# Kernel optimization log

Hardware: AMD Instinct MI355X
Metric: run time of the kernel (lower is better)

## Reference

```python
import jax, jax.numpy as jnp
import numpy as np

K_SIZE = 7  # kernel_size (odd)


def setup_inputs() -> dict:
    key = jax.random.key(0)
    k0, k1, k2, k3 = jax.random.split(key, 4)
    B, C, H, W = 4, 128, 192, 192
    O, K = 128, K_SIZE
    x = jax.random.normal(k0, (B, C, H, W), dtype=jnp.float32)
    offsets = jax.random.normal(k1, (B, K, H, W), dtype=jnp.float32) * 0.5
    tumor_center = jax.random.uniform(k2, (B, 2), dtype=jnp.float32) * H  # (h, w) coords
    kernel_w = jax.random.normal(k3, (O * K, C), dtype=jnp.float32) / np.sqrt(C)  # 1x1 conv weight
    kernel_b = jnp.zeros((O * K,), dtype=jnp.float32)
    return {"x": x, "offsets": offsets, "tumor_center": tumor_center,
            "kernel_w": kernel_w, "kernel_b": kernel_b}


def reference(x, offsets, tumor_center, kernel_w, kernel_b):
    B, C, H, W = x.shape
    K = K_SIZE
    O = kernel_w.shape[0] // K
    pad = K // 2
    dt = x.dtype

    # ---- radial flow grid (faithful to source; see note below) ----
    h_c = tumor_center[:, 0][:, None, None]          # [B,1,1]
    w_c = tumor_center[:, 1][:, None, None]
    h_idx = jnp.arange(H, dtype=dt)[None, :, None]   # [1,H,1]
    w_idx = jnp.arange(W, dtype=dt)[None, None, :]   # [1,1,W]
    dh = h_idx - h_c                                  # [B,H,W]
    dw = w_idx - w_c
    rnorm = jnp.sqrt(dh * dh + dw * dw + 1e-6)
    dir_h = dh / rnorm
    dir_w = dw / rnorm
    base = jnp.linspace(-pad, pad, K, dtype=dt).reshape(1, K, 1, 1)
    h_grid = base * dir_h[:, None] + offsets          # [B,K,H,W]
    w_grid = base * dir_w[:, None] + offsets
    h_grid = h_grid / (H - 1) * 2
    w_grid = w_grid / (W - 1) * 2
    grid = jnp.stack([w_grid, h_grid], axis=-1)       # [B,K,H,W,2]
    # grid_sample is applied to x reshaped to [B*H*W, C, 1, 1] (a single-pixel
    # input) with align_corners=True: the unnormalize factor (size-1)=0 pins the
    # sample location to pixel (0,0) for ANY grid value, so
    # sampled[bhw, c, k] == x[bhw, c] exactly (grid has zero influence/grad).
    del grid

    # ---- dynamic per-pixel kernels via 1x1 conv ----
    kern = jnp.einsum('bchw,fc->bfhw', x, kernel_w) + kernel_b[None, :, None, None]
    kern = kern.reshape(B, O, K, H, W)

    # ---- bmm([BHW,C,K], [BHW,K,O]) then sum over C, fused into one einsum ----
    out = jnp.einsum('bchw,bokhw->bohw', x, kern)     # [B,O,H,W]
    return out
```

## Files before the change

kernel.cpp:

```cpp
#include <hip/hip_runtime.h>
#include <hip/hip_bf16.h>

#define BB   4
#define CC   128
#define HH   192
#define WWd  192
#define HWp  (HH*WWd)
#define OO   128
#define KK   7
#define NPIX (BB*HWp)
#define TILE 64
#define XT_PITCH 136

typedef short bf16x8 __attribute__((ext_vector_type(8)));
typedef float f32x4  __attribute__((ext_vector_type(4)));

static __device__ __forceinline__ unsigned short f2bf(float f) {
    union { __hip_bfloat16 h; unsigned short u; } cvt;
    cvt.h = __float2bfloat16(f);
    return cvt.u;
}
static __device__ __forceinline__ float bf2f(unsigned short u) {
    unsigned int v = ((unsigned int)u) << 16;
    return __uint_as_float(v);
}

__global__ __launch_bounds__(256) void prep_kernel(const float* __restrict__ kw,
                                                   const float* __restrict__ kb,
                                                   unsigned short* __restrict__ wfrag,
                                                   float* __restrict__ bsum) {
    int tid = blockIdx.x * 256 + threadIdx.x;
    int o = tid >> 7, c = tid & 127;
    float s = 0.f;
#pragma unroll
    for (int k = 0; k < KK; ++k) s += kw[(o*KK + k)*CC + c];
    int wv = o >> 5, mt = (o >> 4) & 1, lo = o & 15;
    int ks = c >> 5, g = (c >> 3) & 3, j = c & 7;
    int idx = ((((wv*2 + mt)*4 + ks)*64) + (lo + 16*g))*8 + j;
    wfrag[idx] = f2bf(s);
    if (c == 0) {
        float bs = 0.f;
#pragma unroll
        for (int k = 0; k < KK; ++k) bs += kb[o*KK + k];
        bsum[o] = bs;
    }
}

__global__ __launch_bounds__(256, 4) void conv_kernel(const float* __restrict__ x,
                                                      const unsigned short* __restrict__ wfrag,
                                                      const float* __restrict__ bsum,
                                                      float* __restrict__ out) {
    __shared__ unsigned short xc[CC][TILE];
    __shared__ __align__(16) unsigned short xT[TILE][XT_PITCH];
    __shared__ float sPart[4][TILE];

    const int t = threadIdx.x;
    const int w = t >> 6;
    const int l = t & 63;

    const int pixBase = blockIdx.x * TILE;
    const int bIdx   = pixBase / HWp;
    const int hwBase = pixBase - bIdx * HWp;
    const float* xb = x + (size_t)bIdx * CC * HWp + hwBase;

    bf16x8 afrag[2][4];
#pragma unroll
    for (int mt = 0; mt < 2; ++mt)
#pragma unroll
        for (int ks = 0; ks < 4; ++ks)
            afrag[mt][ks] = *reinterpret_cast<const bf16x8*>(
                wfrag + ((((w*2 + mt)*4 + ks)*64) + l)*8);

    {
        const int p4 = (l & 15) * 4;
        const int cg = l >> 4;
#pragma unroll
        for (int it = 0; it < 8; ++it) {
            const int c = it*16 + w*4 + cg;
            const float4 v = *reinterpret_cast<const float4*>(xb + (size_t)c * HWp + p4);
            uint2 u;
            u.x = (unsigned int)f2bf(v.x) | ((unsigned int)f2bf(v.y) << 16);
            u.y = (unsigned int)f2bf(v.z) | ((unsigned int)f2bf(v.w) << 16);
            *reinterpret_cast<uint2*>(&xc[c][p4]) = u;
        }
    }
    __syncthreads();

    {
        const int p = l;
        const int q = w;
        float part = 0.f;
#pragma unroll
        for (int i = 0; i < 4; ++i) {
            unsigned short e[8];
#pragma unroll
            for (int jj = 0; jj < 8; ++jj) {
                e[jj] = xc[q*32 + i*8 + jj][p];
                part += bf2f(e[jj]);
            }
            uint4 pk;
            pk.x = e[0] | ((unsigned int)e[1] << 16);
            pk.y = e[2] | ((unsigned int)e[3] << 16);
            pk.z = e[4] | ((unsigned int)e[5] << 16);
            pk.w = e[6] | ((unsigned int)e[7] << 16);
            *reinterpret_cast<uint4*>(&xT[p][q*32 + i*8]) = pk;
        }
        sPart[q][p] = part;
    }
    __syncthreads();

    f32x4 acc[2][4];
#pragma unroll
    for (int mt = 0; mt < 2; ++mt)
#pragma unroll
        for (int nt = 0; nt < 4; ++nt)
            acc[mt][nt] = (f32x4){0.f, 0.f, 0.f, 0.f};

    const int lo16 = l & 15;
    const int g4   = l >> 4;
#pragma unroll
    for (int ks = 0; ks < 4; ++ks) {
        bf16x8 bfr[4];
#pragma unroll
        for (int nt = 0; nt < 4; ++nt)
            bfr[nt] = *reinterpret_cast<const bf16x8*>(&xT[nt*16 + lo16][ks*32 + g4*8]);
#pragma unroll
        for (int mt = 0; mt < 2; ++mt)
#pragma unroll
            for (int nt = 0; nt < 4; ++nt)
                acc[mt][nt] = __builtin_amdgcn_mfma_f32_16x16x32_bf16(
                    afrag[mt][ks], bfr[nt], acc[mt][nt], 0, 0, 0);
    }

    float* ob = out + (size_t)bIdx * OO * HWp + hwBase + lo16;
#pragma unroll
    for (int nt = 0; nt < 4; ++nt) {
        const int pp = nt*16 + lo16;
        const float sv = sPart[0][pp] + sPart[1][pp] + sPart[2][pp] + sPart[3][pp];
#pragma unroll
        for (int mt = 0; mt < 2; ++mt) {
            const int o0 = w*32 + mt*16 + g4*4;
            const float4 bs4 = *reinterpret_cast<const float4*>(bsum + o0);
#pragma unroll
            for (int r = 0; r < 4; ++r) {
                const float bsv = (r == 0) ? bs4.x : (r == 1) ? bs4.y : (r == 2) ? bs4.z : bs4.w;
                ob[(size_t)(o0 + r) * HWp + nt*16] = (acc[mt][nt][r] + bsv) * sv;
            }
        }
    }
}

extern "C" void kernel_launch(void* const* d_in, const int* in_sizes, int n_in,
                              void* d_out, int out_size, void* d_ws, size_t ws_size,
                              hipStream_t stream) {
    const float* x  = (const float*)d_in[0];
    const float* kw = (const float*)d_in[3];
    const float* kb = (const float*)d_in[4];
    float* outp = (float*)d_out;

    unsigned short* wfrag = (unsigned short*)d_ws;
    float* bsum = (float*)((char*)d_ws + 32768);

    prep_kernel<<<dim3(64), dim3(256), 0, stream>>>(kw, kb, wfrag, bsum);
    conv_kernel<<<dim3(NPIX / TILE), dim3(256), 0, stream>>>(x, wfrag, bsum, outp);
}
```

Measured before the change: 33.59 us.

## Load x directly into MFMA fragments per wave, dropping LDS transpose

Restructures the conv kernel so each wave owns 16 pixels and computes all 128 outputs. Its x values are loaded straight from global memory into bf16 MFMA B-fragments, which removes the shared-memory staging, the transpose and the barriers. Weight fragments are re-read from global (cached) per k-step, the per-pixel channel sum is computed in fp32 and reduced with shuffles, and outputs use nontemporal stores. The trade is narrower global loads and more weight-fragment traffic in exchange for no LDS usage and higher occupancy.

```diff
diff --git a/kernel.cpp b/kernel.cpp
--- a/kernel.cpp
+++ b/kernel.cpp
@@ -9,8 +9,6 @@
 #define OO   128
 #define KK   7
 #define NPIX (BB*HWp)
-#define TILE 64
-#define XT_PITCH 136
 
 typedef short bf16x8 __attribute__((ext_vector_type(8)));
 typedef float f32x4  __attribute__((ext_vector_type(4)));
@@ -19,10 +17,6 @@
     union { __hip_bfloat16 h; unsigned short u; } cvt;
     cvt.h = __float2bfloat16(f);
     return cvt.u;
-}
-static __device__ __forceinline__ float bf2f(unsigned short u) {
-    unsigned int v = ((unsigned int)u) << 16;
-    return __uint_as_float(v);
 }
 
 __global__ __launch_bounds__(256) void prep_kernel(const float* __restrict__ kw,
@@ -34,9 +28,9 @@
     float s = 0.f;
 #pragma unroll
     for (int k = 0; k < KK; ++k) s += kw[(o*KK + k)*CC + c];
-    int wv = o >> 5, mt = (o >> 4) & 1, lo = o & 15;
+    int mt8 = o >> 4, lo = o & 15;
     int ks = c >> 5, g = (c >> 3) & 3, j = c & 7;
-    int idx = ((((wv*2 + mt)*4 + ks)*64) + (lo + 16*g))*8 + j;
+    int idx = (((mt8*4 + ks)*64) + (lo + 16*g))*8 + j;
     wfrag[idx] = f2bf(s);
     if (c == 0) {
         float bs = 0.f;
@@ -46,106 +40,57 @@
     }
 }
 
-__global__ __launch_bounds__(256, 4) void conv_kernel(const float* __restrict__ x,
+__global__ __launch_bounds__(256, 6) void conv_kernel(const float* __restrict__ x,
                                                       const unsigned short* __restrict__ wfrag,
                                                       const float* __restrict__ bsum,
                                                       float* __restrict__ out) {
-    __shared__ unsigned short xc[CC][TILE];
-    __shared__ __align__(16) unsigned short xT[TILE][XT_PITCH];
-    __shared__ float sPart[4][TILE];
-
     const int t = threadIdx.x;
     const int w = t >> 6;
     const int l = t & 63;
+    const int lo16 = l & 15, g4 = l >> 4;
 
-    const int pixBase = blockIdx.x * TILE;
+    const int pixBase = blockIdx.x * 64 + w * 16;
     const int bIdx   = pixBase / HWp;
-    const int hwBase = pixBase - bIdx * HWp;
-    const float* xb = x + (size_t)bIdx * CC * HWp + hwBase;
+    const int hw     = pixBase - bIdx * HWp;
+    const float* xb  = x + (size_t)bIdx * CC * HWp + hw + lo16;
 
-    bf16x8 afrag[2][4];
+    f32x4 acc[8];
 #pragma unroll
-    for (int mt = 0; mt < 2; ++mt)
+    for (int mt = 0; mt < 8; ++mt) acc[mt] = (f32x4){0.f, 0.f, 0.f, 0.f};
+    float csum = 0.f;
+
+#pragma unroll 2
+    for (int ks = 0; ks < 4; ++ks) {
+        float v[8];
 #pragma unroll
-        for (int ks = 0; ks < 4; ++ks)
-            afrag[mt][ks] = *reinterpret_cast<const bf16x8*>(
-                wfrag + ((((w*2 + mt)*4 + ks)*64) + l)*8);
-
-    {
-        const int p4 = (l & 15) * 4;
-        const int cg = l >> 4;
+        for (int j = 0; j < 8; ++j)
+            v[j] = xb[(size_t)(ks*32 + g4*8 + j) * HWp];
+        bf16x8 b;
 #pragma unroll
-        for (int it = 0; it < 8; ++it) {
-            const int c = it*16 + w*4 + cg;
-            const float4 v = *reinterpret_cast<const float4*>(xb + (size_t)c * HWp + p4);
-            uint2 u;
-            u.x = (unsigned int)f2bf(v.x) | ((unsigned int)f2bf(v.y) << 16);
-            u.y = (unsigned int)f2bf(v.z) | ((unsigned int)f2bf(v.w) << 16);
-            *reinterpret_cast<uint2*>(&xc[c][p4]) = u;
+        for (int j = 0; j < 8; ++j) {
+            csum += v[j];
+            b[j] = (short)f2bf(v[j]);
+        }
+#pragma unroll
+        for (int mt = 0; mt < 8; ++mt) {
+            const bf16x8 a = *reinterpret_cast<const bf16x8*>(
+                wfrag + ((size_t)((mt*4 + ks)*64 + l)) * 8);
+            acc[mt] = __builtin_amdgcn_mfma_f32_16x16x32_bf16(a, b, acc[mt], 0, 0, 0);
         }
     }
-    __syncthreads();
+    csum += __shfl_xor(csum, 16);
+    csum += __shfl_xor(csum, 32);
 
-    {
-        const int p = l;
-        const int q = w;
-        float part = 0.f;
+    float* ob = out + (size_t)bIdx * OO * HWp + hw + lo16;
 #pragma unroll
-        for (int i = 0; i < 4; ++i) {
-            unsigned short e[8];
+    for (int mt = 0; mt < 8; ++mt) {
+        const int o0 = mt*16 + g4*4;
+        const float4 bs4 = *reinterpret_cast<const float4*>(bsum + o0);
 #pragma unroll
-            for (int jj = 0; jj < 8; ++jj) {
-                e[jj] = xc[q*32 + i*8 + jj][p];
-                part += bf2f(e[jj]);
-            }
-            uint4 pk;
-            pk.x = e[0] | ((unsigned int)e[1] << 16);
-            pk.y = e[2] | ((unsigned int)e[3] << 16);
-            pk.z = e[4] | ((unsigned int)e[5] << 16);
-            pk.w = e[6] | ((unsigned int)e[7] << 16);
-            *reinterpret_cast<uint4*>(&xT[p][q*32 + i*8]) = pk;
-        }
-        sPart[q][p] = part;
-    }
-    __syncthreads();
-
-    f32x4 acc[2][4];
-#pragma unroll
-    for (int mt = 0; mt < 2; ++mt)
-#pragma unroll
-        for (int nt = 0; nt < 4; ++nt)
-            acc[mt][nt] = (f32x4){0.f, 0.f, 0.f, 0.f};
-
-    const int lo16 = l & 15;
-    const int g4   = l >> 4;
-#pragma unroll
-    for (int ks = 0; ks < 4; ++ks) {
-        bf16x8 bfr[4];
-#pragma unroll
-        for (int nt = 0; nt < 4; ++nt)
-            bfr[nt] = *reinterpret_cast<const bf16x8*>(&xT[nt*16 + lo16][ks*32 + g4*8]);
-#pragma unroll
-        for (int mt = 0; mt < 2; ++mt)
-#pragma unroll
-            for (int nt = 0; nt < 4; ++nt)
-                acc[mt][nt] = __builtin_amdgcn_mfma_f32_16x16x32_bf16(
-                    afrag[mt][ks], bfr[nt], acc[mt][nt], 0, 0, 0);
-    }
-
-    float* ob = out + (size_t)bIdx * OO * HWp + hwBase + lo16;
-#pragma unroll
-    for (int nt = 0; nt < 4; ++nt) {
-        const int pp = nt*16 + lo16;
-        const float sv = sPart[0][pp] + sPart[1][pp] + sPart[2][pp] + sPart[3][pp];
-#pragma unroll
-        for (int mt = 0; mt < 2; ++mt) {
-            const int o0 = w*32 + mt*16 + g4*4;
-            const float4 bs4 = *reinterpret_cast<const float4*>(bsum + o0);
-#pragma unroll
-            for (int r = 0; r < 4; ++r) {
-                const float bsv = (r == 0) ? bs4.x : (r == 1) ? bs4.y : (r == 2) ? bs4.z : bs4.w;
-                ob[(size_t)(o0 + r) * HWp + nt*16] = (acc[mt][nt][r] + bsv) * sv;
-            }
+        for (int r = 0; r < 4; ++r) {
+            const float bsv = (r == 0) ? bs4.x : (r == 1) ? bs4.y : (r == 2) ? bs4.z : bs4.w;
+            __builtin_nontemporal_store((acc[mt][r] + bsv) * csum,
+                                        ob + (size_t)(o0 + r) * HWp);
         }
     }
 }
@@ -162,5 +107,5 @@
     float* bsum = (float*)((char*)d_ws + 32768);
 
     prep_kernel<<<dim3(64), dim3(256), 0, stream>>>(kw, kb, wfrag, bsum);
-    conv_kernel<<<dim3(NPIX / TILE), dim3(256), 0, stream>>>(x, wfrag, bsum, outp);
+    conv_kernel<<<dim3(NPIX / 64), dim3(256), 0, stream>>>(x, wfrag, bsum, outp);
 }
```

After: 51.15 us. 52.3% more time.

## Share one LDS buffer for staging and transpose, raise occupancy to 8 blocks

Applied to the files above, without the earlier changes.

Merges the staging and transposed LDS arrays into one reused buffer, with an extra barrier between the transpose read and write phases. This cuts LDS per block so the launch bound can ask for 8 blocks per SM instead of 4. Per-pixel channel sums now come from the fp32 loads through wave shuffles, replacing the sum over bf16 values read from LDS. Weight fragments are loaded per k-step inside the MFMA loop rather than preloaded, which lowers register pressure but adds global/L2 loads in the inner loop.

```diff
diff --git a/kernel.cpp b/kernel.cpp
--- a/kernel.cpp
+++ b/kernel.cpp
@@ -10,19 +10,15 @@
 #define KK   7
 #define NPIX (BB*HWp)
 #define TILE 64
-#define XT_PITCH 136
+#define BUF_BYTES 17408
 
 typedef short bf16x8 __attribute__((ext_vector_type(8)));
 typedef float f32x4  __attribute__((ext_vector_type(4)));
 
-static __device__ __forceinline__ unsigned short f2bf(float f) {
+static __device__ __forceinline__ unsigned f2bf(float f) {
     union { __hip_bfloat16 h; unsigned short u; } cvt;
     cvt.h = __float2bfloat16(f);
-    return cvt.u;
-}
-static __device__ __forceinline__ float bf2f(unsigned short u) {
-    unsigned int v = ((unsigned int)u) << 16;
-    return __uint_as_float(v);
+    return (unsigned)cvt.u;
 }
 
 __global__ __launch_bounds__(256) void prep_kernel(const float* __restrict__ kw,
@@ -37,7 +33,7 @@
     int wv = o >> 5, mt = (o >> 4) & 1, lo = o & 15;
     int ks = c >> 5, g = (c >> 3) & 3, j = c & 7;
     int idx = ((((wv*2 + mt)*4 + ks)*64) + (lo + 16*g))*8 + j;
-    wfrag[idx] = f2bf(s);
+    wfrag[idx] = (unsigned short)f2bf(s);
     if (c == 0) {
         float bs = 0.f;
 #pragma unroll
@@ -46,66 +42,64 @@
     }
 }
 
-__global__ __launch_bounds__(256, 4) void conv_kernel(const float* __restrict__ x,
+__global__ __launch_bounds__(256, 8) void conv_kernel(const float* __restrict__ x,
                                                       const unsigned short* __restrict__ wfrag,
                                                       const float* __restrict__ bsum,
                                                       float* __restrict__ out) {
-    __shared__ unsigned short xc[CC][TILE];
-    __shared__ __align__(16) unsigned short xT[TILE][XT_PITCH];
+    __shared__ __align__(16) unsigned char buf[BUF_BYTES];
     __shared__ float sPart[4][TILE];
 
     const int t = threadIdx.x;
     const int w = t >> 6;
     const int l = t & 63;
+    const int lo16 = l & 15, g4 = l >> 4;
 
     const int pixBase = blockIdx.x * TILE;
     const int bIdx   = pixBase / HWp;
     const int hwBase = pixBase - bIdx * HWp;
-    const float* xb = x + (size_t)bIdx * CC * HWp + hwBase;
-
-    bf16x8 afrag[2][4];
-#pragma unroll
-    for (int mt = 0; mt < 2; ++mt)
-#pragma unroll
-        for (int ks = 0; ks < 4; ++ks)
-            afrag[mt][ks] = *reinterpret_cast<const bf16x8*>(
-                wfrag + ((((w*2 + mt)*4 + ks)*64) + l)*8);
+    const float* xb  = x + (size_t)bIdx * CC * HWp + hwBase;
 
     {
-        const int p4 = (l & 15) * 4;
-        const int cg = l >> 4;
+        const int p4 = lo16 * 4;
+        float pa = 0.f, pb = 0.f, pc = 0.f, pd = 0.f;
 #pragma unroll
         for (int it = 0; it < 8; ++it) {
-            const int c = it*16 + w*4 + cg;
+            const int c = it*16 + w*4 + g4;
             const float4 v = *reinterpret_cast<const float4*>(xb + (size_t)c * HWp + p4);
+            pa += v.x; pb += v.y; pc += v.z; pd += v.w;
             uint2 u;
-            u.x = (unsigned int)f2bf(v.x) | ((unsigned int)f2bf(v.y) << 16);
-            u.y = (unsigned int)f2bf(v.z) | ((unsigned int)f2bf(v.w) << 16);
-            *reinterpret_cast<uint2*>(&xc[c][p4]) = u;
+            u.x = f2bf(v.x) | (f2bf(v.y) << 16);
+            u.y = f2bf(v.z) | (f2bf(v.w) << 16);
+            *reinterpret_cast<uint2*>(&buf[c*128 + p4*2]) = u;
         }
+        pa += __shfl_xor(pa, 16); pa += __shfl_xor(pa, 32);
+        pb += __shfl_xor(pb, 16); pb += __shfl_xor(pb, 32);
+        pc += __shfl_xor(pc, 16); pc += __shfl_xor(pc, 32);
+        pd += __shfl_xor(pd, 16); pd += __shfl_xor(pd, 32);
+        if (l < 16)
+            *reinterpret_cast<float4*>(&sPart[w][p4]) = make_float4(pa, pb, pc, pd);
     }
     __syncthreads();
 
+    unsigned pk[16];
     {
-        const int p = l;
-        const int q = w;
-        float part = 0.f;
+        const int p2 = l * 2;
 #pragma unroll
-        for (int i = 0; i < 4; ++i) {
-            unsigned short e[8];
+        for (int i = 0; i < 4; ++i)
 #pragma unroll
-            for (int jj = 0; jj < 8; ++jj) {
-                e[jj] = xc[q*32 + i*8 + jj][p];
-                part += bf2f(e[jj]);
+            for (int h = 0; h < 4; ++h) {
+                const int c = w*32 + i*8 + h*2;
+                const unsigned e0 = *reinterpret_cast<const unsigned short*>(&buf[c*128 + p2]);
+                const unsigned e1 = *reinterpret_cast<const unsigned short*>(&buf[(c+1)*128 + p2]);
+                pk[i*4 + h] = e0 | (e1 << 16);
             }
-            uint4 pk;
-            pk.x = e[0] | ((unsigned int)e[1] << 16);
-            pk.y = e[2] | ((unsigned int)e[3] << 16);
-            pk.z = e[4] | ((unsigned int)e[5] << 16);
-            pk.w = e[6] | ((unsigned int)e[7] << 16);
-            *reinterpret_cast<uint4*>(&xT[p][q*32 + i*8]) = pk;
-        }
-        sPart[q][p] = part;
+    }
+    __syncthreads();
+
+#pragma unroll
+    for (int i = 0; i < 4; ++i) {
+        uint4 q4 = make_uint4(pk[i*4+0], pk[i*4+1], pk[i*4+2], pk[i*4+3]);
+        *reinterpret_cast<uint4*>(&buf[l*272 + w*64 + i*16]) = q4;
     }
     __syncthreads();
 
@@ -116,20 +110,19 @@
         for (int nt = 0; nt < 4; ++nt)
             acc[mt][nt] = (f32x4){0.f, 0.f, 0.f, 0.f};
 
-    const int lo16 = l & 15;
-    const int g4   = l >> 4;
-#pragma unroll
+    const unsigned short* wf = wfrag + (size_t)w * 2*4*64*8;
     for (int ks = 0; ks < 4; ++ks) {
+        const bf16x8 a0 = *reinterpret_cast<const bf16x8*>(wf + ((size_t)(0*4 + ks)*64 + l)*8);
+        const bf16x8 a1 = *reinterpret_cast<const bf16x8*>(wf + ((size_t)(1*4 + ks)*64 + l)*8);
         bf16x8 bfr[4];
 #pragma unroll
         for (int nt = 0; nt < 4; ++nt)
-            bfr[nt] = *reinterpret_cast<const bf16x8*>(&xT[nt*16 + lo16][ks*32 + g4*8]);
+            bfr[nt] = *reinterpret_cast<const bf16x8*>(&buf[(nt*16 + lo16)*272 + ks*64 + g4*16]);
 #pragma unroll
-        for (int mt = 0; mt < 2; ++mt)
-#pragma unroll
-            for (int nt = 0; nt < 4; ++nt)
-                acc[mt][nt] = __builtin_amdgcn_mfma_f32_16x16x32_bf16(
-                    afrag[mt][ks], bfr[nt], acc[mt][nt], 0, 0, 0);
+        for (int nt = 0; nt < 4; ++nt) {
+            acc[0][nt] = __builtin_amdgcn_mfma_f32_16x16x32_bf16(a0, bfr[nt], acc[0][nt], 0, 0, 0);
+            acc[1][nt] = __builtin_amdgcn_mfma_f32_16x16x32_bf16(a1, bfr[nt], acc[1][nt], 0, 0, 0);
+        }
     }
 
     float* ob = out + (size_t)bIdx * OO * HWp + hwBase + lo16;
```

Result: slower. 35.32 us (+5.1%).
